# Kernel tuning notes

Measured on AMD Instinct MI355X. Metric: run time of the kernel, lower is better.

The kernel has to match this reference:

```python
import jax, jax.numpy as jnp
import numpy as np
from functools import partial

B = 8192
BS = 6           # board_size
NSQ = BS * BS    # 36
FLAT = 128 * NSQ # 4608
EPS = 1e-5


def _conv(x, w, b):
    # x: (N,C,H,W), w: (O,I,3,3), SAME padding
    y = jax.lax.conv_general_dilated(x, w, (1, 1), 'SAME',
                                     dimension_numbers=('NCHW', 'OIHW', 'NCHW'))
    return y + b[None, :, None, None]


def _bn_eval(x, g, b, m, v):
    inv = jax.lax.rsqrt(v + EPS)
    return (x - m[None, :, None, None]) * (g * inv)[None, :, None, None] + b[None, :, None, None]


def _ln(x, g, b):
    mu = jnp.mean(x, axis=-1, keepdims=True)
    var = jnp.mean(jnp.square(x - mu), axis=-1, keepdims=True)
    return (x - mu) * jax.lax.rsqrt(var + EPS) * g + b


def _lin(x, w, b):
    return x @ w.T + b


def setup_inputs() -> dict:
    key = jax.random.key(0)
    ks = iter(jax.random.split(key, 64))
    nrm = lambda shape, s=0.05: jax.random.normal(next(ks), shape, jnp.float32) * s
    d = {}
    d['x'] = jax.random.normal(next(ks), (B, 4, BS, BS), jnp.float32)
    d['conv1_w'] = nrm((64, 4, 3, 3)); d['conv1_b'] = nrm((64,))
    d['bn1_g'] = jnp.ones((64,)); d['bn1_b'] = jnp.zeros((64,))
    d['bn1_m'] = nrm((64,)); d['bn1_v'] = jnp.ones((64,))
    d['conv2_w'] = nrm((128, 64, 3, 3)); d['conv2_b'] = nrm((128,))
    d['bn2_g'] = jnp.ones((128,)); d['bn2_b'] = jnp.zeros((128,))
    d['bn2_m'] = nrm((128,)); d['bn2_v'] = jnp.ones((128,))
    d['conv3_w'] = nrm((128, 128, 3, 3)); d['conv3_b'] = nrm((128,))
    d['bn3_g'] = jnp.ones((128,)); d['bn3_b'] = jnp.zeros((128,))
    d['bn3_m'] = nrm((128,)); d['bn3_v'] = jnp.ones((128,))
    d['pfc1_w'] = nrm((256, FLAT)); d['pfc1_b'] = nrm((256,))
    d['pln_g'] = jnp.ones((256,)); d['pln_b'] = jnp.zeros((256,))
    d['pfc2_w'] = nrm((NSQ, 256)); d['pfc2_b'] = nrm((NSQ,))
    d['mfc1_w'] = nrm((256, FLAT + NSQ)); d['mfc1_b'] = nrm((256,))
    d['mln_g'] = jnp.ones((256,)); d['mln_b'] = jnp.zeros((256,))
    d['mfc2_w'] = nrm((NSQ, 256)); d['mfc2_b'] = nrm((NSQ,))
    d['vfc1_w'] = nrm((256, FLAT)); d['vfc1_b'] = nrm((256,))
    d['vln_g'] = jnp.ones((256,)); d['vln_b'] = jnp.zeros((256,))
    d['vfc2_w'] = nrm((1, 256)); d['vfc2_b'] = nrm((1,))
    return d


def reference(x, conv1_w, conv1_b, bn1_g, bn1_b, bn1_m, bn1_v,
              conv2_w, conv2_b, bn2_g, bn2_b, bn2_m, bn2_v,
              conv3_w, conv3_b, bn3_g, bn3_b, bn3_m, bn3_v,
              pfc1_w, pfc1_b, pln_g, pln_b, pfc2_w, pfc2_b,
              mfc1_w, mfc1_b, mln_g, mln_b, mfc2_w, mfc2_b,
              vfc1_w, vfc1_b, vln_g, vln_b, vfc2_w, vfc2_b):
    h = jax.nn.relu(_bn_eval(_conv(x, conv1_w, conv1_b), bn1_g, bn1_b, bn1_m, bn1_v))
    h = jax.nn.relu(_bn_eval(_conv(h, conv2_w, conv2_b), bn2_g, bn2_b, bn2_m, bn2_v))
    h = jax.nn.relu(_bn_eval(_conv(h, conv3_w, conv3_b), bn3_g, bn3_b, bn3_m, bn3_v))
    feats = h.reshape(-1, FLAT)  # (B, 4608)

    piece_h = jax.nn.relu(_ln(_lin(feats, pfc1_w, pfc1_b), pln_g, pln_b))
    piece_logits = _lin(piece_h, pfc2_w, pfc2_b)  # (B, 36)

    # eval-mode: one-hot of argmax piece
    sel = jax.nn.one_hot(jnp.argmax(piece_logits, axis=1), NSQ, dtype=feats.dtype)
    move_in = jnp.concatenate([feats, sel], axis=1)  # (B, 4644)
    move_h = jax.nn.relu(_ln(_lin(move_in, mfc1_w, mfc1_b), mln_g, mln_b))
    move_logits = _lin(move_h, mfc2_w, mfc2_b)  # (B, 36)

    val_h = jax.nn.relu(_ln(_lin(feats, vfc1_w, vfc1_b), vln_g, vln_b))
    val = _lin(val_h, vfc2_w, vfc2_b)  # (B, 1)

    piece_adv = piece_logits - jnp.mean(piece_logits, axis=1, keepdims=True)
    move_adv = move_logits - jnp.mean(move_logits, axis=1, keepdims=True)

    # action_idx = i*36 + j  ->  fused outer-sum broadcast, reshape to (B, 1296)
    q = val[:, :, None] + piece_adv[:, :, None] + move_adv[:, None, :]
    return q.reshape(-1, NSQ * NSQ)
```

## Files before the change

### kernel.cpp

```cpp
#include <hip/hip_runtime.h>
#include <hip/hip_bf16.h>

#define BQ 8192
#define CHUNK 2048
#define NCHUNK 4
typedef __attribute__((ext_vector_type(8))) __bf16 bf16x8;
typedef __attribute__((ext_vector_type(4))) float f32x4;
typedef __attribute__((ext_vector_type(4))) int int4v;

__device__ __forceinline__ f32x4 mfma16(bf16x8 a, bf16x8 b, f32x4 c) {
    return __builtin_amdgcn_mfma_f32_16x16x32_bf16(a, b, c, 0, 0, 0);
}

__device__ __forceinline__ void split3(float v, __hip_bfloat16& s0,
                                       __hip_bfloat16& s1, __hip_bfloat16& s2) {
    s0 = __float2bfloat16(v);
    float r = v - __bfloat162float(s0);
    s1 = __float2bfloat16(r);
    r -= __bfloat162float(s1);
    s2 = __float2bfloat16(r);
}

__device__ __forceinline__ int pair_a(int pp) { return (0x211000 >> (4 * pp)) & 0xF; }
__device__ __forceinline__ int pair_w(int pp) { return (0x010210 >> (4 * pp)) & 0xF; }


__global__ void prep_scalars_k(
    const float* __restrict__ c1b, const float* __restrict__ g1,
    const float* __restrict__ b1,  const float* __restrict__ m1,
    const float* __restrict__ v1,
    const float* __restrict__ c2b, const float* __restrict__ g2,
    const float* __restrict__ b2,  const float* __restrict__ m2,
    const float* __restrict__ v2,
    const float* __restrict__ c3b, const float* __restrict__ g3,
    const float* __restrict__ b3,  const float* __restrict__ m3,
    const float* __restrict__ v3,
    const float* __restrict__ pfb, const float* __restrict__ vfb,
    const float* __restrict__ mfb,
    float* __restrict__ scale1, float* __restrict__ bias1f,
    float* __restrict__ scale2, float* __restrict__ bias2f,
    float* __restrict__ scale3, float* __restrict__ bias3f,
    float* __restrict__ biasfc)
{
    int t = threadIdx.x;
    if (t < 64) {
        float s = g1[t] * rsqrtf(v1[t] + 1e-5f);
        scale1[t] = s;
        bias1f[t] = (c1b[t] - m1[t]) * s + b1[t];
    }
    if (t < 128) {
        float s2 = g2[t] * rsqrtf(v2[t] + 1e-5f);
        scale2[t] = s2;
        bias2f[t] = (c2b[t] - m2[t]) * s2 + b2[t];
        float s3 = g3[t] * rsqrtf(v3[t] + 1e-5f);
        scale3[t] = s3;
        bias3f[t] = (c3b[t] - m3[t]) * s3 + b3[t];
    }
    if (t < 256)      biasfc[t] = pfb[t];
    else if (t < 512) biasfc[t] = vfb[t - 256];
    else              biasfc[t] = mfb[t - 512];
}

template<int CIN>
__global__ void prep_convw_k(const float* __restrict__ w,
                             __hip_bfloat16* __restrict__ wt, size_t planeW)
{
    int id = blockIdx.x * 256 + threadIdx.x;
    int kk = id & 31;
    int n  = (id >> 5) & 127;
    int kt = id >> 12;
    int k  = kt * 32 + kk;
    int s  = k / CIN;
    int i  = k & (CIN - 1);
    __hip_bfloat16 s0, s1, s2;
    split3(w[(n * CIN + i) * 9 + s], s0, s1, s2);
    size_t dest = (size_t)kt * 4096 + ((n >> 5) * 1024) + (((n >> 4) & 1) * 512)
                + ((kk >> 3) * 128) + ((n & 15) * 8) + (kk & 7);
    wt[dest] = s0; wt[dest + planeW] = s1; wt[dest + 2 * planeW] = s2;
}

__global__ void prep_bigw_k(const float* __restrict__ pw,
                            const float* __restrict__ vw,
                            const float* __restrict__ mw,
                            __hip_bfloat16* __restrict__ bigw, size_t planeBW)
{
    int id = blockIdx.x * 256 + threadIdx.x;
    int kk = id & 31;
    int n  = (id >> 5) % 768;
    int kt = id / (32 * 768);
    int k2 = kt * 32 + kk;
    int c  = k2 & 127, p = k2 >> 7;
    int k  = c * 36 + p;
    float v;
    if (n < 256)      v = pw[n * 4608 + k];
    else if (n < 512) v = vw[(n - 256) * 4608 + k];
    else              v = mw[(n - 512) * 4644 + k];
    __hip_bfloat16 s0, s1, s2;
    split3(v, s0, s1, s2);
    size_t dest = (size_t)kt * 24576 + ((n >> 7) * 4096) + (((n >> 6) & 1) * 2048)
                + (((n >> 4) & 3) * 512) + ((kk >> 3) * 128) + ((n & 15) * 8) + (kk & 7);
    bigw[dest] = s0; bigw[dest + planeBW] = s1; bigw[dest + 2 * planeBW] = s2;
}

__global__ void prep_selw_k(const float* __restrict__ mw,
                            float* __restrict__ selw)
{
    int j = blockIdx.x, d = threadIdx.x;
    selw[j * 256 + d] = mw[d * 4644 + 4608 + j];
}


__global__ __launch_bounds__(256)
void conv1_k(const float* __restrict__ x,
             const float* __restrict__ w,
             const float* __restrict__ scale, const float* __restrict__ biasf,
             __hip_bfloat16* __restrict__ out, size_t planeA,
             int b_base)
{
    __shared__ float wl[64 * 37];
    int tid = threadIdx.x;
    for (int c = tid; c < 64 * 36; c += 256) {
        int o = c / 36, k = c - o * 36;
        wl[o * 37 + k] = w[c];
    }
    __syncthreads();
    unsigned gid = blockIdx.x * 256 + tid;
    int o = gid & 63;
    unsigned bp = gid >> 6;
    unsigned b = bp / 36;
    int p = bp - b * 36;
    int py = p / 6, px = p - py * 6;
    const float* xb = x + (size_t)(b_base + b) * 4 * 36;
    float acc = 0.f;
#pragma unroll
    for (int i = 0; i < 4; ++i) {
#pragma unroll
        for (int s = 0; s < 9; ++s) {
            int ny = py + s / 3 - 1, nx = px + s % 3 - 1;
            if ((unsigned)ny < 6u && (unsigned)nx < 6u)
                acc += xb[i * 36 + ny * 6 + nx] * wl[o * 37 + i * 9 + s];
        }
    }
    float v = fmaxf(acc * scale[o] + biasf[o], 0.f);
    __hip_bfloat16 s0, s1, s2;
    split3(v, s0, s1, s2);
    size_t idx = (size_t)bp * 64 + o;
    out[idx] = s0; out[idx + planeA] = s1; out[idx + 2 * planeA] = s2;
}

template<int CIN>
__global__ __launch_bounds__(256, 2)
void conv_gemm_k(const __hip_bfloat16* __restrict__ in, size_t planeA,
                 const __hip_bfloat16* __restrict__ wt, size_t planeW,
                 const float* __restrict__ scale,
                 const float* __restrict__ biasf,
                 __hip_bfloat16* __restrict__ out, size_t planeO)
{
    constexpr int PS  = CIN + 8;
    constexpr int CPB = CIN / 32;
    constexpr int NSLICE = CPB * 9;
    constexpr int XS_ELEMS = 144 * PS;
    __shared__ __align__(16) __hip_bfloat16 smem[XS_ELEMS + CIN];
    __hip_bfloat16* xs = smem;

    const int tid  = threadIdx.x;
    const int wave = tid >> 6, lane = tid & 63;
    const int m16  = lane & 15, quad = lane >> 4;
    const int b0   = blockIdx.x * 4;

    if (tid < CIN) smem[XS_ELEMS + tid] = __float2bfloat16(0.f);

    f32x4 acc[9][2];
#pragma unroll
    for (int i = 0; i < 9; ++i) { acc[i][0] = f32x4{0,0,0,0}; acc[i][1] = f32x4{0,0,0,0}; }

    const int bo0 = wave * 1024 + lane * 8;
    const int bo1 = bo0 + 512;

    constexpr int CHPP = CIN / 8;
    for (int pp = 0; pp < 6; ++pp) {
        const __hip_bfloat16* inb = in + (size_t)pair_a(pp) * planeA + (size_t)b0 * 36 * CIN;
        const __hip_bfloat16* wP  = wt + (size_t)pair_w(pp) * planeW;
        const bool stage_x = (pp == 0) || (pair_a(pp) != pair_a(pp - 1));

        if (stage_x) {
            __syncthreads();
            for (int c = tid; c < 144 * CHPP; c += 256) {
                int pix = c / CHPP;
                int off = (c - pix * CHPP) * 8;
                *(int4v*)(xs + pix * PS + off) = *(const int4v*)(inb + pix * CIN + off);
            }
            __syncthreads();
        }

        bf16x8 wc0 = *(const bf16x8*)(wP + bo0);
        bf16x8 wc1 = *(const bf16x8*)(wP + bo1);

        for (int s = 0; s < 9; ++s) {
            const int dy = s / 3 - 1, dx = s % 3 - 1;
            int aoff[9];
#pragma unroll
            for (int rt = 0; rt < 9; ++rt) {
                int m   = rt * 16 + m16;
                int img = m / 36;
                int p   = m - img * 36;
                int py  = p / 6, px = p - py * 6;
                int ny  = py + dy, nx = px + dx;
                bool ok = ((unsigned)ny < 6u) && ((unsigned)nx < 6u);
                int base = ok ? ((img * 36 + ny * 6 + nx) * PS) : XS_ELEMS;
                aoff[rt] = base + quad * 8;
            }
#pragma unroll
            for (int c = 0; c < CPB; ++c) {
                const int kt = s * CPB + c;
                const int ktn = (kt + 1 < NSLICE) ? (kt + 1) : 0;
                const __hip_bfloat16* wN = wP + (size_t)ktn * 4096;
                bf16x8 wn0 = *(const bf16x8*)(wN + bo0);
                bf16x8 wn1 = *(const bf16x8*)(wN + bo1);
                const int coff = c * 32;
#pragma unroll
                for (int rt = 0; rt < 9; ++rt) {
                    bf16x8 af = *(const bf16x8*)(smem + aoff[rt] + coff);
                    acc[rt][0] = mfma16(af, wc0, acc[rt][0]);
                    acc[rt][1] = mfma16(af, wc1, acc[rt][1]);
                }
                wc0 = wn0; wc1 = wn1;
            }
        }
    }

#pragma unroll
    for (int ct = 0; ct < 2; ++ct) {
        const int n = wave * 32 + ct * 16 + m16;
        const float sc = scale[n], bi = biasf[n];
#pragma unroll
        for (int rt = 0; rt < 9; ++rt) {
            const int mrow = rt * 16 + quad * 4;
#pragma unroll
            for (int r = 0; r < 4; ++r) {
                float v = fmaxf(acc[rt][ct][r] * sc + bi, 0.f);
                __hip_bfloat16 s0, s1, s2;
                split3(v, s0, s1, s2);
                size_t idx = (size_t)(b0 * 36 + mrow + r) * 128 + n;
                out[idx] = s0; out[idx + planeO] = s1; out[idx + 2 * planeO] = s2;
            }
        }
    }
}


__global__ __launch_bounds__(256, 3)
void fc_partial_k(const __hip_bfloat16* __restrict__ A, size_t planeF,
                  const __hip_bfloat16* __restrict__ Bw, size_t planeBW,
                  float* __restrict__ partial)
{
    constexpr int HBUF = 4096;
    __shared__ __align__(16) __hip_bfloat16 smem[2 * 2 * HBUF];
    const int tid = threadIdx.x, wave = tid >> 6, lane = tid & 63;
    const int m16 = lane & 15, quad = lane >> 4;
    const int mblk = blockIdx.x & 15;
    const int rest = blockIdx.x >> 4;
    const int nblk = rest % 6;
    const int pp   = rest / 6;
    const size_t m0 = (size_t)mblk * 128;
    const int wr = wave >> 1, wc = wave & 1;

    const __hip_bfloat16* Ap = A + (size_t)pair_a(pp) * planeF;
    const __hip_bfloat16* Bp = Bw + (size_t)pair_w(pp) * planeBW + (size_t)nblk * 4096;

    f32x4 acc[4][4];
#pragma unroll
    for (int i = 0; i < 4; ++i)
#pragma unroll
        for (int j = 0; j < 4; ++j) acc[i][j] = f32x4{0,0,0,0};

    const int cr = tid >> 2, co = (tid & 3) * 8;
    int ao[4], bo[4];
#pragma unroll
    for (int i = 0; i < 4; ++i) {
        ao[i] = wr * 2048 + i * 512 + lane * 8;
        bo[i] = HBUF + wc * 2048 + i * 512 + lane * 8;
    }
    const int adst = ((cr >> 4) & 3) * 512 + (tid & 3) * 128 + (cr & 15) * 8;

    auto ldA = [&](int kt, int4v& a0, int4v& a1) {
        const __hip_bfloat16* base = Ap + (m0 + cr) * 4608 + kt * 32 + co;
        a0 = *(const int4v*)base;
        a1 = *(const int4v*)(base + (size_t)64 * 4608);
    };
    auto ldB = [&](int kt, int4v& b0, int4v& b1) {
        const int4v* g = (const int4v*)(Bp + (size_t)kt * 24576);
        b0 = g[tid]; b1 = g[tid + 256];
    };
    auto stAB = [&](int buf, int4v a0, int4v a1, int4v b0, int4v b1) {
        __hip_bfloat16* base = smem + buf * 2 * HBUF;
        *(int4v*)(base + adst) = a0;
        *(int4v*)(base + 2048 + adst) = a1;
        *(int4v*)(base + HBUF + tid * 8) = b0;
        *(int4v*)(base + HBUF + (tid + 256) * 8) = b1;
    };

    { int4v a0,a1,b0,b1; ldA(0,a0,a1); ldB(0,b0,b1); stAB(0,a0,a1,b0,b1); }
    __syncthreads();
    int cur = 0;

    for (int kt = 0; kt < 144; ++kt) {
        int4v a0, a1, b0, b1;
        const bool more = (kt < 143);
        if (more) { ldA(kt + 1, a0, a1); ldB(kt + 1, b0, b1); }
        const __hip_bfloat16* base = smem + cur * 2 * HBUF;
        bf16x8 af[4], bf[4];
#pragma unroll
        for (int i = 0; i < 4; ++i) {
            af[i] = *(const bf16x8*)(base + ao[i]);
            bf[i] = *(const bf16x8*)(base + bo[i]);
        }
#pragma unroll
        for (int i = 0; i < 4; ++i)
#pragma unroll
            for (int j = 0; j < 4; ++j)
                acc[i][j] = mfma16(af[i], bf[j], acc[i][j]);
        if (more) { stAB(cur ^ 1, a0, a1, b0, b1); }
        __syncthreads();
        cur ^= 1;
    }

    float* outp = partial + (size_t)pp * CHUNK * 768;
    const int n0 = nblk * 128;
#pragma unroll
    for (int i = 0; i < 4; ++i) {
        const int row = wr * 64 + i * 16 + quad * 4;
#pragma unroll
        for (int j = 0; j < 4; ++j) {
            const int col = n0 + wc * 64 + j * 16 + m16;
#pragma unroll
            for (int r = 0; r < 4; ++r)
                outp[(m0 + row + r) * 768 + col] = acc[i][j][r];
        }
    }
}


__global__ __launch_bounds__(256)
void heads_k(const float* __restrict__ partial,
             const float* __restrict__ biasfc,
             const float* __restrict__ pln_g, const float* __restrict__ pln_b,
             const float* __restrict__ pfc2_w, const float* __restrict__ pfc2_b,
             const float* __restrict__ mln_g, const float* __restrict__ mln_b,
             const float* __restrict__ mfc2_w, const float* __restrict__ mfc2_b,
             const float* __restrict__ vln_g, const float* __restrict__ vln_b,
             const float* __restrict__ vfc2_w, const float* __restrict__ vfc2_b,
             const float* __restrict__ selw,
             float* __restrict__ q,
             int b_base)
{
    __shared__ float hp[256], hv[256], hm[256];
    __shared__ float pl[36], ml[36];
    __shared__ float red[4];
    __shared__ float valv, plm_s, mlm_s;
    __shared__ int amax_s;

    const int tid = threadIdx.x, wave = tid >> 6, lane = tid & 63;
    const size_t b = blockIdx.x;
    const size_t bg = b_base + b;

    float pp = biasfc[tid], vv = biasfc[256 + tid], mm = biasfc[512 + tid];
#pragma unroll
    for (int k = 0; k < 6; ++k) {
        const float* row = partial + (size_t)k * CHUNK * 768 + b * 768;
        pp += row[tid]; vv += row[256 + tid]; mm += row[512 + tid];
    }

    auto warpSum = [&](float v) {
        v += __shfl_xor(v, 1);  v += __shfl_xor(v, 2);  v += __shfl_xor(v, 4);
        v += __shfl_xor(v, 8);  v += __shfl_xor(v, 16); v += __shfl_xor(v, 32);
        return v;
    };
    auto blockSum = [&](float v) {
        v = warpSum(v);
        if (lane == 0) red[wave] = v;
        __syncthreads();
        float s = red[0] + red[1] + red[2] + red[3];
        __syncthreads();
        return s;
    };
    auto lnrelu = [&](float x, const float* g, const float* bb) {
        float mu  = blockSum(x) * (1.f / 256.f);
        float d   = x - mu;
        float var = blockSum(d * d) * (1.f / 256.f);
        float y   = d * rsqrtf(var + 1e-5f) * g[tid] + bb[tid];
        return fmaxf(y, 0.f);
    };

    hp[tid] = lnrelu(pp, pln_g, pln_b);
    hv[tid] = lnrelu(vv, vln_g, vln_b);
    __syncthreads();

    {
        float h0 = hp[lane], h1 = hp[64 + lane], h2 = hp[128 + lane], h3 = hp[192 + lane];
#pragma unroll
        for (int jj = 0; jj < 9; ++jj) {
            int j = wave * 9 + jj;
            const float* wr_ = pfc2_w + j * 256;
            float s = h0 * wr_[lane] + h1 * wr_[64 + lane]
                    + h2 * wr_[128 + lane] + h3 * wr_[192 + lane];
            s = warpSum(s);
            if (lane == 0) pl[j] = s + pfc2_b[j];
        }
        if (wave == 0) {
            float g0 = hv[lane], g1 = hv[64 + lane], g2 = hv[128 + lane], g3 = hv[192 + lane];
            float s = g0 * vfc2_w[lane] + g1 * vfc2_w[64 + lane]
                    + g2 * vfc2_w[128 + lane] + g3 * vfc2_w[192 + lane];
            s = warpSum(s);
            if (lane == 0) valv = s + vfc2_b[0];
        }
    }
    __syncthreads();
    if (tid == 0) {
        float m = -1e30f, s = 0.f; int idx = 0;
        for (int j = 0; j < 36; ++j) { float v = pl[j]; s += v; if (v > m) { m = v; idx = j; } }
        plm_s = s * (1.f / 36.f); amax_s = idx;
    }
    __syncthreads();

    mm += selw[amax_s * 256 + tid];
    hm[tid] = lnrelu(mm, mln_g, mln_b);
    __syncthreads();
    {
        float h0 = hm[lane], h1 = hm[64 + lane], h2 = hm[128 + lane], h3 = hm[192 + lane];
#pragma unroll
        for (int jj = 0; jj < 9; ++jj) {
            int j = wave * 9 + jj;
            const float* wr_ = mfc2_w + j * 256;
            float s = h0 * wr_[lane] + h1 * wr_[64 + lane]
                    + h2 * wr_[128 + lane] + h3 * wr_[192 + lane];
            s = warpSum(s);
            if (lane == 0) ml[j] = s + mfc2_b[j];
        }
    }
    __syncthreads();
    if (tid == 0) {
        float s = 0.f;
        for (int j = 0; j < 36; ++j) s += ml[j];
        mlm_s = s * (1.f / 36.f);
    }
    __syncthreads();

    const float val = valv, plm = plm_s, mlm = mlm_s;
    for (int idx = tid; idx < 1296; idx += 256) {
        int i = idx / 36, j = idx - i * 36;
        q[bg * 1296 + idx] = val + (pl[i] - plm) + (ml[j] - mlm);
    }
}


extern "C" void kernel_launch(void* const* d_in, const int* in_sizes, int n_in,
                              void* d_out, int out_size, void* d_ws, size_t ws_size,
                              hipStream_t stream)
{
    const float* x       = (const float*)d_in[0];
    const float* conv1_w = (const float*)d_in[1];
    const float* conv1_b = (const float*)d_in[2];
    const float* bn1_g   = (const float*)d_in[3];
    const float* bn1_b   = (const float*)d_in[4];
    const float* bn1_m   = (const float*)d_in[5];
    const float* bn1_v   = (const float*)d_in[6];
    const float* conv2_w = (const float*)d_in[7];
    const float* conv2_b = (const float*)d_in[8];
    const float* bn2_g   = (const float*)d_in[9];
    const float* bn2_b   = (const float*)d_in[10];
    const float* bn2_m   = (const float*)d_in[11];
    const float* bn2_v   = (const float*)d_in[12];
    const float* conv3_w = (const float*)d_in[13];
    const float* conv3_b = (const float*)d_in[14];
    const float* bn3_g   = (const float*)d_in[15];
    const float* bn3_b   = (const float*)d_in[16];
    const float* bn3_m   = (const float*)d_in[17];
    const float* bn3_v   = (const float*)d_in[18];
    const float* pfc1_w  = (const float*)d_in[19];
    const float* pfc1_b  = (const float*)d_in[20];
    const float* pln_g   = (const float*)d_in[21];
    const float* pln_b   = (const float*)d_in[22];
    const float* pfc2_w  = (const float*)d_in[23];
    const float* pfc2_b  = (const float*)d_in[24];
    const float* mfc1_w  = (const float*)d_in[25];
    const float* mfc1_b  = (const float*)d_in[26];
    const float* mln_g   = (const float*)d_in[27];
    const float* mln_b   = (const float*)d_in[28];
    const float* mfc2_w  = (const float*)d_in[29];
    const float* mfc2_b  = (const float*)d_in[30];
    const float* vfc1_w  = (const float*)d_in[31];
    const float* vfc1_b  = (const float*)d_in[32];
    const float* vln_g   = (const float*)d_in[33];
    const float* vln_b   = (const float*)d_in[34];
    const float* vfc2_w  = (const float*)d_in[35];
    const float* vfc2_b  = (const float*)d_in[36];

    const size_t planeW2 = 576 * 128;
    const size_t planeW3 = 1152 * 128;
    const size_t planeBW = (size_t)4608 * 768;
    const size_t planeA1 = (size_t)CHUNK * 36 * 64;
    const size_t planeA2 = (size_t)CHUNK * 36 * 128;

    char* ws = (char*)d_ws;
    size_t off = 0;
    auto alloc = [&](size_t bytes) -> char* {
        char* p = ws + off; off += (bytes + 255) & ~(size_t)255; return p;
    };
    __hip_bfloat16* w2t  = (__hip_bfloat16*)alloc(3 * planeW2 * 2);
    __hip_bfloat16* w3t  = (__hip_bfloat16*)alloc(3 * planeW3 * 2);
    __hip_bfloat16* bigw = (__hip_bfloat16*)alloc(3 * planeBW * 2);
    float* selw   = (float*)alloc(36 * 256 * 4);
    float* scale1 = (float*)alloc(64 * 4);
    float* bias1f = (float*)alloc(64 * 4);
    float* scale2 = (float*)alloc(128 * 4);
    float* bias2f = (float*)alloc(128 * 4);
    float* scale3 = (float*)alloc(128 * 4);
    float* bias3f = (float*)alloc(128 * 4);
    float* biasfc = (float*)alloc(768 * 4);
    char* A1 = alloc(3 * planeA2 * 2);
    char* A2 = alloc(3 * planeA2 * 2);

    prep_scalars_k<<<1, 768, 0, stream>>>(
        conv1_b, bn1_g, bn1_b, bn1_m, bn1_v,
        conv2_b, bn2_g, bn2_b, bn2_m, bn2_v,
        conv3_b, bn3_g, bn3_b, bn3_m, bn3_v,
        pfc1_b, vfc1_b, mfc1_b,
        scale1, bias1f, scale2, bias2f, scale3, bias3f, biasfc);
    prep_convw_k<64><<<288, 256, 0, stream>>>(conv2_w, w2t, planeW2);
    prep_convw_k<128><<<576, 256, 0, stream>>>(conv3_w, w3t, planeW3);
    prep_bigw_k<<<13824, 256, 0, stream>>>(pfc1_w, vfc1_w, mfc1_w, bigw, planeBW);
    prep_selw_k<<<36, 256, 0, stream>>>(mfc1_w, selw);

    __hip_bfloat16* h1s  = (__hip_bfloat16*)A1;
    __hip_bfloat16* h2s  = (__hip_bfloat16*)A2;
    __hip_bfloat16* h3s  = (__hip_bfloat16*)A1;
    float*          fpar = (float*)A2;

    for (int cchunk = 0; cchunk < NCHUNK; ++cchunk) {
        const int b_base = cchunk * CHUNK;
        conv1_k<<<CHUNK * 36 * 64 / 256, 256, 0, stream>>>(
            x, conv1_w, scale1, bias1f, h1s, planeA1, b_base);
        conv_gemm_k<64><<<CHUNK / 4, 256, 0, stream>>>(
            h1s, planeA1, w2t, planeW2, scale2, bias2f, h2s, planeA2);
        conv_gemm_k<128><<<CHUNK / 4, 256, 0, stream>>>(
            h2s, planeA2, w3t, planeW3, scale3, bias3f, h3s, planeA2);
        fc_partial_k<<<576, 256, 0, stream>>>(h3s, planeA2, bigw, planeBW, fpar);
        heads_k<<<CHUNK, 256, 0, stream>>>(fpar, biasfc,
            pln_g, pln_b, pfc2_w, pfc2_b,
            mln_g, mln_b, mfc2_w, mfc2_b,
            vln_g, vln_b, vfc2_w, vfc2_b,
            selw, (float*)d_out, b_base);
    }
}
```

Before: 1.764 ms.

## Split FC GEMM over K, load B fragments directly to registers

The fc_partial kernel now splits the 144-step K loop into two halves, doubling the grid to 1152 blocks and writing 12 partial planes that heads_k sums. B operand fragments are loaded straight from global memory into registers with a two-deep register prefetch instead of being staged through shared memory, which halves LDS usage. The aim is better occupancy and latency hiding for the big FC GEMM. The cost is a larger partial buffer and extra reduction traffic in heads_k, plus more register pressure from the prefetched B fragments.

Result: faster. 1.728 ms (-2.0%).

```diff
diff --git a/kernel.cpp b/kernel.cpp
--- a/kernel.cpp
+++ b/kernel.cpp
@@ -254,14 +254,17 @@
                   const __hip_bfloat16* __restrict__ Bw, size_t planeBW,
                   float* __restrict__ partial)
 {
-    constexpr int HBUF = 4096;
-    __shared__ __align__(16) __hip_bfloat16 smem[2 * 2 * HBUF];
+    constexpr int ABUF = 4096;
+    __shared__ __align__(16) __hip_bfloat16 smem[2 * ABUF];
     const int tid = threadIdx.x, wave = tid >> 6, lane = tid & 63;
     const int m16 = lane & 15, quad = lane >> 4;
     const int mblk = blockIdx.x & 15;
-    const int rest = blockIdx.x >> 4;
+    int rest = blockIdx.x >> 4;
     const int nblk = rest % 6;
-    const int pp   = rest / 6;
+    rest /= 6;
+    const int pp = rest % 6;
+    const int ks = rest / 6;
+    const int kt0 = ks * 72, ktend = kt0 + 72;
     const size_t m0 = (size_t)mblk * 128;
     const int wr = wave >> 1, wc = wave & 1;
 
@@ -275,12 +278,10 @@
         for (int j = 0; j < 4; ++j) acc[i][j] = f32x4{0,0,0,0};
 
     const int cr = tid >> 2, co = (tid & 3) * 8;
-    int ao[4], bo[4];
-#pragma unroll
-    for (int i = 0; i < 4; ++i) {
-        ao[i] = wr * 2048 + i * 512 + lane * 8;
-        bo[i] = HBUF + wc * 2048 + i * 512 + lane * 8;
-    }
+    int ao[4];
+#pragma unroll
+    for (int i = 0; i < 4; ++i) ao[i] = wr * 2048 + i * 512 + lane * 8;
+    const int bofs = wc * 2048 + lane * 8;
     const int adst = ((cr >> 4) & 3) * 512 + (tid & 3) * 128 + (cr & 15) * 8;
 
     auto ldA = [&](int kt, int4v& a0, int4v& a1) {
@@ -288,44 +289,56 @@
         a0 = *(const int4v*)base;
         a1 = *(const int4v*)(base + (size_t)64 * 4608);
     };
-    auto ldB = [&](int kt, int4v& b0, int4v& b1) {
-        const int4v* g = (const int4v*)(Bp + (size_t)kt * 24576);
-        b0 = g[tid]; b1 = g[tid + 256];
-    };
-    auto stAB = [&](int buf, int4v a0, int4v a1, int4v b0, int4v b1) {
-        __hip_bfloat16* base = smem + buf * 2 * HBUF;
+    auto ldB = [&](int kt, bf16x8* bf) {
+        const __hip_bfloat16* base = Bp + (size_t)kt * 24576 + bofs;
+#pragma unroll
+        for (int i = 0; i < 4; ++i) bf[i] = *(const bf16x8*)(base + i * 512);
+    };
+    auto stA = [&](int buf, int4v a0, int4v a1) {
+        __hip_bfloat16* base = smem + buf * ABUF;
         *(int4v*)(base + adst) = a0;
         *(int4v*)(base + 2048 + adst) = a1;
-        *(int4v*)(base + HBUF + tid * 8) = b0;
-        *(int4v*)(base + HBUF + (tid + 256) * 8) = b1;
-    };
-
-    { int4v a0,a1,b0,b1; ldA(0,a0,a1); ldB(0,b0,b1); stAB(0,a0,a1,b0,b1); }
+    };
+
+    int4v pa, pb, qa, qb;
+    bf16x8 bfc[4], bf1[4];
+    {
+        int4v a0, a1;
+        ldA(kt0, a0, a1);
+        ldB(kt0, bfc);
+        ldA(kt0 + 1, pa, pb);
+        ldB(kt0 + 1, bf1);
+        stA(0, a0, a1);
+    }
     __syncthreads();
     int cur = 0;
 
-    for (int kt = 0; kt < 144; ++kt) {
-        int4v a0, a1, b0, b1;
-        const bool more = (kt < 143);
-        if (more) { ldA(kt + 1, a0, a1); ldB(kt + 1, b0, b1); }
-        const __hip_bfloat16* base = smem + cur * 2 * HBUF;
-        bf16x8 af[4], bf[4];
-#pragma unroll
-        for (int i = 0; i < 4; ++i) {
-            af[i] = *(const bf16x8*)(base + ao[i]);
-            bf[i] = *(const bf16x8*)(base + bo[i]);
-        }
+#pragma unroll 2
+    for (int kt = kt0; kt < ktend; ++kt) {
+        const int ktn = (kt + 2 < ktend) ? (kt + 2) : kt0;
+        bf16x8 bfn[4];
+        ldA(ktn, qa, qb);
+        ldB(ktn, bfn);
+        const __hip_bfloat16* base = smem + cur * ABUF;
+        bf16x8 af[4];
+#pragma unroll
+        for (int i = 0; i < 4; ++i) af[i] = *(const bf16x8*)(base + ao[i]);
 #pragma unroll
         for (int i = 0; i < 4; ++i)
 #pragma unroll
             for (int j = 0; j < 4; ++j)
-                acc[i][j] = mfma16(af[i], bf[j], acc[i][j]);
-        if (more) { stAB(cur ^ 1, a0, a1, b0, b1); }
+                acc[i][j] = mfma16(af[i], bfc[j], acc[i][j]);
+        if (kt + 1 < ktend) stA(cur ^ 1, pa, pb);
         __syncthreads();
         cur ^= 1;
-    }
-
-    float* outp = partial + (size_t)pp * CHUNK * 768;
+        pa = qa; pb = qb;
+#pragma unroll
+        for (int i = 0; i < 4; ++i) bfc[i] = bf1[i];
+#pragma unroll
+        for (int i = 0; i < 4; ++i) bf1[i] = bfn[i];
+    }
+
+    float* outp = partial + (size_t)rest * CHUNK * 768;
     const int n0 = nblk * 128;
 #pragma unroll
     for (int i = 0; i < 4; ++i) {
@@ -366,7 +379,7 @@
 
     float pp = biasfc[tid], vv = biasfc[256 + tid], mm = biasfc[512 + tid];
 #pragma unroll
-    for (int k = 0; k < 6; ++k) {
+    for (int k = 0; k < 12; ++k) {
         const float* row = partial + (size_t)k * CHUNK * 768 + b * 768;
         pp += row[tid]; vv += row[256 + tid]; mm += row[512 + tid];
     }
@@ -519,7 +532,7 @@
     float* bias3f = (float*)alloc(128 * 4);
     float* biasfc = (float*)alloc(768 * 4);
     char* A1 = alloc(3 * planeA2 * 2);
-    char* A2 = alloc(3 * planeA2 * 2);
+    char* A2 = alloc((size_t)12 * CHUNK * 768 * 4);
 
     prep_scalars_k<<<1, 768, 0, stream>>>(
         conv1_b, bn1_g, bn1_b, bn1_m, bn1_v,
@@ -545,7 +558,7 @@
             h1s, planeA1, w2t, planeW2, scale2, bias2f, h2s, planeA2);
         conv_gemm_k<128><<<CHUNK / 4, 256, 0, stream>>>(
             h2s, planeA2, w3t, planeW3, scale3, bias3f, h3s, planeA2);
-        fc_partial_k<<<576, 256, 0, stream>>>(h3s, planeA2, bigw, planeBW, fpar);
+        fc_partial_k<<<1152, 256, 0, stream>>>(h3s, planeA2, bigw, planeBW, fpar);
         heads_k<<<CHUNK, 256, 0, stream>>>(fpar, biasfc,
             pln_g, pln_b, pfc2_w, pfc2_b,
             mln_g, mln_b, mfc2_w, mfc2_b,
```
